# Optimization experiments

Hardware: AMD Instinct MI355X
Metric: run time of the kernel (lower is better)

Reference implementation:

```python
import jax, jax.numpy as jnp
import numpy as np

DIM = 1024
N_HEAD = 16
HEAD_DIM = DIM // N_HEAD
HIDDEN = 4 * DIM
EPS = 1e-6
NEG = -1e9


def setup_inputs() -> dict:
    key = jax.random.key(0)
    ks = jax.random.split(key, 9)
    B, T = 2, 2048
    x = jax.random.normal(ks[0], (B, T, DIM), dtype=jnp.float32)
    # additive causal mask [T, T]
    mask = jnp.where(jnp.tril(jnp.ones((T, T), dtype=bool)), 0.0, NEG).astype(jnp.float32)
    s = 0.02
    wq = jax.random.normal(ks[1], (DIM, DIM), dtype=jnp.float32) * s
    wk = jax.random.normal(ks[2], (DIM, DIM), dtype=jnp.float32) * s
    wv = jax.random.normal(ks[3], (DIM, DIM), dtype=jnp.float32) * s
    wo = jax.random.normal(ks[4], (DIM, DIM), dtype=jnp.float32) * s
    w1 = jax.random.normal(ks[5], (DIM, HIDDEN), dtype=jnp.float32) * s
    w2 = jax.random.normal(ks[6], (HIDDEN, DIM), dtype=jnp.float32) * s
    g_attn = jnp.ones((DIM,), dtype=jnp.float32)
    g_ffn = jnp.ones((DIM,), dtype=jnp.float32)
    return {"x": x, "mask": mask, "wq": wq, "wk": wk, "wv": wv, "wo": wo,
            "w1": w1, "w2": w2, "g_attn": g_attn, "g_ffn": g_ffn}


def _rmsnorm(x, g):
    norm = jax.lax.rsqrt(jnp.mean(jnp.square(x), axis=-1, keepdims=True) + EPS)
    return (x * norm) * g


def _attention(x, mask, wq, wk, wv, wo):
    B, T, C = x.shape
    # project and split heads: [B, H, T, D]
    q = (x @ wq).reshape(B, T, N_HEAD, HEAD_DIM).transpose(0, 2, 1, 3)
    k = (x @ wk).reshape(B, T, N_HEAD, HEAD_DIM).transpose(0, 2, 1, 3)
    v = (x @ wv).reshape(B, T, N_HEAD, HEAD_DIM).transpose(0, 2, 1, 3)
    attn = jnp.einsum('bhtd,bhsd->bhts', q, k) / np.sqrt(HEAD_DIM).astype(np.float32)
    attn = attn + mask  # broadcast [T,T] over [B,H,T,T]
    p = jax.nn.softmax(attn, axis=-1)
    out = jnp.einsum('bhts,bhsd->bhtd', p, v)
    out = out.transpose(0, 2, 1, 3).reshape(B, T, C)
    return out @ wo


def reference(x, mask, wq, wk, wv, wo, w1, w2, g_attn, g_ffn):
    x = x + _attention(_rmsnorm(x, g_attn), mask, wq, wk, wv, wo)
    h = _rmsnorm(x, g_ffn)
    return x + (jax.nn.silu(h @ w1) @ w2)
```

## Files before the change

kernel.cpp:

```cpp
#include <hip/hip_runtime.h>
#include <hip/hip_bf16.h>
#include <cstdint>
#include <cstddef>

#define DIM    1024
#define NHEAD  16
#define HDIM   64
#define HIDDEN 4096
#define TSEQ   2048
#define TOKENS 4096

typedef __attribute__((ext_vector_type(4))) float  f32x4;
typedef __attribute__((ext_vector_type(8))) short  short8;
typedef __attribute__((ext_vector_type(8))) __bf16 bf16x8;

__device__ __forceinline__ short f2bf(float f) {
    union { float f; uint32_t u; } v; v.f = f;
    uint32_t u = v.u;
    uint32_t r = (u + 0x7fffu + ((u >> 16) & 1u)) >> 16;
    return (short)r;
}

__device__ __forceinline__ float bf2f(short s) {
    uint32_t u = ((uint32_t)(uint16_t)s) << 16;
    return __builtin_bit_cast(float, u);
}

__device__ __forceinline__ f32x4 mfma_bf16(short8 a, short8 b, f32x4 c) {
    return __builtin_amdgcn_mfma_f32_16x16x32_bf16(
        __builtin_bit_cast(bf16x8, a), __builtin_bit_cast(bf16x8, b), c, 0, 0, 0);
}

__device__ __forceinline__ void barrier_lds() {
    asm volatile("s_waitcnt lgkmcnt(0)\n\ts_barrier" ::: "memory");
}

__global__ __launch_bounds__(256) void transpose_w(
    const float* __restrict__ W, short* __restrict__ Wt, int K, int N)
{
    __shared__ float tile[64][65];
    const int tid = threadIdx.x;
    const int n0 = blockIdx.x * 64, k0 = blockIdx.y * 64;
    for (int i = tid; i < 4096; i += 256) {
        int r = i >> 6, c = i & 63;
        tile[r][c] = W[(size_t)(k0 + r) * N + n0 + c];
    }
    __syncthreads();
    for (int i = tid; i < 4096; i += 256) {
        int r = i >> 6, c = i & 63;
        Wt[(size_t)(n0 + r) * K + k0 + c] = f2bf(tile[c][r]);
    }
}

__global__ __launch_bounds__(256) void transpose_v(
    const short* __restrict__ qkv, short* __restrict__ Vt)
{
    __shared__ short tile[64][72];
    const int tid = threadIdx.x;
    const int s0 = blockIdx.x * 64, bh = blockIdx.y;
    const int b = bh >> 4, h = bh & 15;
    const short* src = qkv + ((size_t)(b * TSEQ + s0)) * 3072 + 2048 + h * 64;
    for (int i = tid; i < 512; i += 256) {
        int r = i >> 3, cg = i & 7;
        *(short8*)&tile[r][cg * 8] = *(const short8*)(src + (size_t)r * 3072 + cg * 8);
    }
    __syncthreads();
    short* dst = Vt + ((size_t)bh * 64) * TSEQ + s0;
    for (int i = tid; i < 512; i += 256) {
        int d = i >> 3, sg = i & 7;
        short8 o;
#pragma unroll
        for (int j = 0; j < 8; ++j) o[j] = tile[sg * 8 + j][d];
        *(short8*)(dst + (size_t)d * TSEQ + sg * 8) = o;
    }
}

__global__ __launch_bounds__(256) void rmsnorm_k(
    const float* __restrict__ x, const float* __restrict__ g, short* __restrict__ out)
{
    const int t = blockIdx.x, tid = threadIdx.x;
    const int wave = tid >> 6, lane = tid & 63;
    const float4 v = ((const float4*)(x + (size_t)t * DIM))[tid];
    float ss = v.x * v.x + v.y * v.y + v.z * v.z + v.w * v.w;
#pragma unroll
    for (int d = 1; d < 64; d <<= 1) ss += __shfl_xor(ss, d, 64);
    __shared__ float red[4];
    if (lane == 0) red[wave] = ss;
    __syncthreads();
    float tot = red[0] + red[1] + red[2] + red[3];
    float rn = rsqrtf(tot * (1.0f / (float)DIM) + 1e-6f);
    const float4 gv = ((const float4*)g)[tid];
    short4 ov = make_short4(f2bf(v.x * rn * gv.x), f2bf(v.y * rn * gv.y),
                            f2bf(v.z * rn * gv.z), f2bf(v.w * rn * gv.w));
    ((short4*)(out + (size_t)t * DIM))[tid] = ov;
}

template <int EPI>
__global__ __launch_bounds__(256) void gemm_bt(
    const short* __restrict__ A, const short* __restrict__ Bt,
    void* __restrict__ Cout, const float* __restrict__ res,
    int M, int N, int K)
{
    __shared__ short As[128 * 64];
    __shared__ short Bs[128 * 64];
    const int tid  = threadIdx.x;
    const int wave = tid >> 6, lane = tid & 63;
    const int lm = lane & 15, quad = lane >> 4;
    const int wm = wave & 1, wn = wave >> 1;
    const int m0 = blockIdx.x * 128, n0 = blockIdx.y * 128;
    const int Ksl = K / gridDim.z;
    const int kbeg = blockIdx.z * Ksl;
    const int nIter = Ksl >> 6;

    const f32x4 zero = {0.f, 0.f, 0.f, 0.f};
    f32x4 acc[4][4];
#pragma unroll
    for (int i = 0; i < 4; ++i)
#pragma unroll
        for (int j = 0; j < 4; ++j) acc[i][j] = zero;

    const int srow = tid >> 3;
    const int scol = (tid & 7) * 8;
    const int pcol = ((tid & 7) ^ (srow & 7)) * 8;
    const short* Ap = A + (size_t)(m0 + srow) * K + kbeg + scol;
    const short* Bp = Bt + (size_t)(n0 + srow) * K + kbeg + scol;

    short8 ar[4], br[4];

    auto loadtile = [&]() {
#pragma unroll
        for (int j = 0; j < 4; ++j) {
            ar[j] = *(const short8*)(Ap + (size_t)(j * 32) * K);
            br[j] = *(const short8*)(Bp + (size_t)(j * 32) * K);
        }
        Ap += 64; Bp += 64;
    };

    auto storetile = [&]() {
#pragma unroll
        for (int j = 0; j < 4; ++j) {
            *(short8*)&As[(srow + j * 32) * 64 + pcol] = ar[j];
            *(short8*)&Bs[(srow + j * 32) * 64 + pcol] = br[j];
        }
    };

    const int e = lm & 7;
    auto compute = [&]() {
#pragma unroll
        for (int kk = 0; kk < 2; ++kk) {
            short8 af[4], bf[4];
#pragma unroll
            for (int mt = 0; mt < 4; ++mt)
                af[mt] = *(const short8*)&As[(wm * 64 + mt * 16 + lm) * 64 +
                                             ((((kk << 2) | quad) ^ e) << 3)];
#pragma unroll
            for (int nt = 0; nt < 4; ++nt)
                bf[nt] = *(const short8*)&Bs[(wn * 64 + nt * 16 + lm) * 64 +
                                             ((((kk << 2) | quad) ^ e) << 3)];
#pragma unroll
            for (int mt = 0; mt < 4; ++mt)
#pragma unroll
                for (int nt = 0; nt < 4; ++nt)
                    acc[mt][nt] = mfma_bf16(af[mt], bf[nt], acc[mt][nt]);
        }
    };

    loadtile();

    for (int it = 0; it < nIter; ++it) {
        barrier_lds();
        storetile();
        barrier_lds();
        if (it + 1 < nIter) loadtile();
        compute();
    }

#pragma unroll
    for (int mt = 0; mt < 4; ++mt) {
#pragma unroll
        for (int r = 0; r < 4; ++r) {
            const int row = m0 + wm * 64 + mt * 16 + quad * 4 + r;
#pragma unroll
            for (int nt = 0; nt < 4; ++nt) {
                const int col = n0 + wn * 64 + nt * 16 + lm;
                const size_t idx = (size_t)row * N + col;
                const float v = acc[mt][nt][r];
                if constexpr (EPI == 0) {
                    ((short*)Cout)[idx] = f2bf(v);
                } else if constexpr (EPI == 1) {
                    ((float*)Cout)[idx] = res[idx] + v;
                } else if constexpr (EPI == 2) {
                    ((short*)Cout)[idx] = f2bf(v / (1.0f + __expf(-v)));
                } else {
                    ((short*)Cout)[(size_t)blockIdx.z * M * N + idx] = f2bf(v);
                }
            }
        }
    }
}

__global__ __launch_bounds__(256) void combine_k4(
    const short* __restrict__ p, const float* __restrict__ res,
    float* __restrict__ out, int n)
{
    const int i = blockIdx.x * 256 + threadIdx.x;
    if (i * 4 < n) {
        float4 v = ((const float4*)res)[i];
#pragma unroll
        for (int s = 0; s < 4; ++s) {
            short4 ps = ((const short4*)(p + (size_t)s * n))[i];
            v.x += bf2f(ps.x); v.y += bf2f(ps.y);
            v.z += bf2f(ps.z); v.w += bf2f(ps.w);
        }
        ((float4*)out)[i] = v;
    }
}

__global__ __launch_bounds__(256) void combine_rms4(
    const short* __restrict__ p, const float* __restrict__ res,
    const float* __restrict__ g, float* __restrict__ x2out,
    short* __restrict__ nout)
{
    const int t = blockIdx.x, tid = threadIdx.x;
    const int wave = tid >> 6, lane = tid & 63;
    const size_t i4 = (size_t)t * 256 + tid;
    float4 v = ((const float4*)res)[i4];
#pragma unroll
    for (int s = 0; s < 4; ++s) {
        short4 ps = ((const short4*)(p + (size_t)s * TOKENS * DIM))[i4];
        v.x += bf2f(ps.x); v.y += bf2f(ps.y);
        v.z += bf2f(ps.z); v.w += bf2f(ps.w);
    }
    ((float4*)x2out)[i4] = v;
    float ss = v.x * v.x + v.y * v.y + v.z * v.z + v.w * v.w;
#pragma unroll
    for (int d = 1; d < 64; d <<= 1) ss += __shfl_xor(ss, d, 64);
    __shared__ float red[4];
    if (lane == 0) red[wave] = ss;
    __syncthreads();
    float tot = red[0] + red[1] + red[2] + red[3];
    float rn = rsqrtf(tot * (1.0f / (float)DIM) + 1e-6f);
    const float4 gv = ((const float4*)g)[tid];
    short4 ov = make_short4(f2bf(v.x * rn * gv.x), f2bf(v.y * rn * gv.y),
                            f2bf(v.z * rn * gv.z), f2bf(v.w * rn * gv.w));
    ((short4*)nout)[i4] = ov;
}

#define PLP 72
__global__ __launch_bounds__(256, 2) void attn_k(
    const short* __restrict__ qkv, const short* __restrict__ Vt,
    short* __restrict__ out)
{
    __shared__ short Ks[2][64 * 64];
    __shared__ short Vts[2][64 * 64];
    __shared__ short Ps[4][32 * PLP];

    const int tid = threadIdx.x, wave = tid >> 6, lane = tid & 63;
    const int pair = wave >> 1, wv = wave & 1;
    const int lm = lane & 15, quad = lane >> 4;
    const int e = lm & 7;
    const int bh = blockIdx.x;
    const int qt = (gridDim.y - 1) - blockIdx.y;
    const int b = bh >> 4, h = bh & 15;
    const int q0 = qt * 64;

    const int n  = qt + 1;
    const int nA = (n + 1) >> 1;
    const int nP = pair ? (n >> 1) : nA;
    const int sbase = pair ? nA : 0;

    const int tp = tid & 127;
    const int rr = tp >> 3, cg = tp & 7;
    const int pcol = (cg ^ (rr & 7)) * 8;

    const short* qb = qkv + ((size_t)(b * TSEQ + q0)) * 3072 + h * 64;
    short8 aq[2][2];
#pragma unroll
    for (int mt = 0; mt < 2; ++mt)
#pragma unroll
        for (int kk = 0; kk < 2; ++kk)
            aq[mt][kk] = *(const short8*)(qb + (size_t)(wv * 32 + mt * 16 + lm) * 3072 + kk * 32 + quad * 8);

    const short* kb  = qkv + (size_t)b * TSEQ * 3072 + 1024 + h * 64;
    const short* vtb = Vt + (size_t)bh * 64 * TSEQ;

    const short ONEBF = (short)0x3F80;
    const short8 ones8 = {ONEBF, ONEBF, ONEBF, ONEBF, ONEBF, ONEBF, ONEBF, ONEBF};

    const f32x4 zero = {0.f, 0.f, 0.f, 0.f};
    f32x4 o_acc[2][4];
    f32x4 lacc[2];
#pragma unroll
    for (int mt = 0; mt < 2; ++mt) {
#pragma unroll
        for (int t = 0; t < 4; ++t) o_acc[mt][t] = zero;
        lacc[mt] = zero;
    }

    short8 kr[4], vr[4];
    if (nP > 0) {
        const size_t s0i = (size_t)sbase * 64;
#pragma unroll
        for (int j = 0; j < 4; ++j) {
            kr[j] = *(const short8*)(kb + (s0i + rr + j * 16) * 3072 + cg * 8);
            vr[j] = *(const short8*)(vtb + (size_t)(rr + j * 16) * TSEQ + s0i + cg * 8);
        }
    }

    for (int it = 0; it < nA; ++it) {
        const int st = sbase + it;
        const bool act = it < nP;
        __syncthreads();
        if (act) {
#pragma unroll
            for (int j = 0; j < 4; ++j) {
                *(short8*)&Ks[pair][(rr + j * 16) * 64 + pcol] = kr[j];
                *(short8*)&Vts[pair][(rr + j * 16) * 64 + pcol] = vr[j];
            }
        }
        __syncthreads();
        if (act && it + 1 < nP) {
            const size_t sn = (size_t)(st + 1) * 64;
#pragma unroll
            for (int j = 0; j < 4; ++j) {
                kr[j] = *(const short8*)(kb + (sn + rr + j * 16) * 3072 + cg * 8);
                vr[j] = *(const short8*)(vtb + (size_t)(rr + j * 16) * TSEQ + sn + cg * 8);
            }
        }
        if (!act) continue;

        f32x4 sa[2][4];
#pragma unroll
        for (int mt = 0; mt < 2; ++mt)
#pragma unroll
            for (int nt = 0; nt < 4; ++nt) sa[mt][nt] = zero;
#pragma unroll
        for (int kk = 0; kk < 2; ++kk) {
#pragma unroll
            for (int nt = 0; nt < 4; ++nt) {
                short8 bk = *(const short8*)&Ks[pair][(nt * 16 + lm) * 64 +
                                                     ((((kk << 2) | quad) ^ e) << 3)];
                sa[0][nt] = mfma_bf16(aq[0][kk], bk, sa[0][nt]);
                sa[1][nt] = mfma_bf16(aq[1][kk], bk, sa[1][nt]);
            }
        }

        const int s0 = st * 64;
        if (st != qt) {
#pragma unroll
            for (int mt = 0; mt < 2; ++mt)
#pragma unroll
                for (int nt = 0; nt < 4; ++nt)
#pragma unroll
                    for (int r = 0; r < 4; ++r) {
                        float p = exp2f(0.18033688011112042f * sa[mt][nt][r]);
                        Ps[wave][(mt * 16 + quad * 4 + r) * PLP + nt * 16 + lm] =
                            (short)(__builtin_bit_cast(uint32_t, p) >> 16);
                    }
        } else {
#pragma unroll
            for (int mt = 0; mt < 2; ++mt) {
                const int qrow = q0 + wv * 32 + mt * 16 + quad * 4;
#pragma unroll
                for (int nt = 0; nt < 4; ++nt) {
                    const int col = s0 + nt * 16 + lm;
#pragma unroll
                    for (int r = 0; r < 4; ++r) {
                        float p = exp2f(0.18033688011112042f * sa[mt][nt][r]);
                        if (col > qrow + r) p = 0.f;
                        Ps[wave][(mt * 16 + quad * 4 + r) * PLP + nt * 16 + lm] =
                            (short)(__builtin_bit_cast(uint32_t, p) >> 16);
                    }
                }
            }
        }

#pragma unroll
        for (int kk = 0; kk < 2; ++kk) {
            short8 ap0 = *(const short8*)&Ps[wave][lm * PLP + kk * 32 + quad * 8];
            short8 ap1 = *(const short8*)&Ps[wave][(16 + lm) * PLP + kk * 32 + quad * 8];
            lacc[0] = mfma_bf16(ap0, ones8, lacc[0]);
            lacc[1] = mfma_bf16(ap1, ones8, lacc[1]);
#pragma unroll
            for (int t = 0; t < 4; ++t) {
                short8 bv = *(const short8*)&Vts[pair][(t * 16 + lm) * 64 +
                                                       ((((kk << 2) | quad) ^ e) << 3)];
                o_acc[0][t] = mfma_bf16(ap0, bv, o_acc[0][t]);
                o_acc[1][t] = mfma_bf16(ap1, bv, o_acc[1][t]);
            }
        }
    }

    __syncthreads();
    float* Ob = (float*)&Ks[0][0];
    float* Lb = (float*)&Ps[0][0];
    if (pair == 1) {
#pragma unroll
        for (int mt = 0; mt < 2; ++mt)
#pragma unroll
            for (int t = 0; t < 4; ++t)
#pragma unroll
                for (int r = 0; r < 4; ++r)
                    Ob[(wv * 32 + mt * 16 + quad * 4 + r) * 64 + t * 16 + lm] = o_acc[mt][t][r];
        if (lm == 0) {
#pragma unroll
            for (int mt = 0; mt < 2; ++mt)
#pragma unroll
                for (int r = 0; r < 4; ++r)
                    Lb[wv * 32 + mt * 16 + quad * 4 + r] = lacc[mt][r];
        }
    }
    __syncthreads();
    if (pair == 0) {
#pragma unroll
        for (int mt = 0; mt < 2; ++mt) {
#pragma unroll
            for (int r = 0; r < 4; ++r) {
                const int lrow = wv * 32 + mt * 16 + quad * 4 + r;
                float ltot = lacc[mt][r] + Lb[lrow];
                const float inv = 1.0f / ltot;
                const int token = b * TSEQ + q0 + lrow;
#pragma unroll
                for (int t = 0; t < 4; ++t) {
                    float o = o_acc[mt][t][r] + Ob[lrow * 64 + t * 16 + lm];
                    out[(size_t)token * 1024 + h * 64 + t * 16 + lm] = f2bf(o * inv);
                }
            }
        }
    }
}

extern "C" void kernel_launch(void* const* d_in, const int* in_sizes, int n_in,
                              void* d_out, int out_size, void* d_ws, size_t ws_size,
                              hipStream_t stream)
{
    const float* x      = (const float*)d_in[0];
    const float* wq     = (const float*)d_in[2];
    const float* wk     = (const float*)d_in[3];
    const float* wv     = (const float*)d_in[4];
    const float* wo     = (const float*)d_in[5];
    const float* w1     = (const float*)d_in[6];
    const float* w2     = (const float*)d_in[7];
    const float* g_attn = (const float*)d_in[8];
    const float* g_ffn  = (const float*)d_in[9];
    float* out = (float*)d_out;

    char* ws = (char*)d_ws;
    const size_t MB = 1024 * 1024;
    short* Wqkv_t = (short*)(ws + 0);
    short* Wo_t   = (short*)(ws + 6 * MB);
    short* W1_t   = (short*)(ws + 8 * MB);
    short* xn     = (short*)(ws + 16 * MB);
    short* hbuf   = (short*)(ws + 24 * MB);
    short* qkv    = (short*)(ws + 32 * MB);
    short* pbufO  = (short*)(ws + 32 * MB);
    short* Vt     = (short*)(ws + 64 * MB);
    float* x2     = (float*)(ws + 64 * MB);
    short* W2_t   = (short*)(ws + 80 * MB);
    short* pbuf2  = (short*)(ws + 0);

    dim3 blk(256);

    transpose_w<<<dim3(16, 16), blk, 0, stream>>>(wq, Wqkv_t, 1024, 1024);
    transpose_w<<<dim3(16, 16), blk, 0, stream>>>(wk, Wqkv_t + (size_t)1024 * 1024, 1024, 1024);
    transpose_w<<<dim3(16, 16), blk, 0, stream>>>(wv, Wqkv_t + (size_t)2048 * 1024, 1024, 1024);
    transpose_w<<<dim3(16, 16), blk, 0, stream>>>(wo, Wo_t, 1024, 1024);
    transpose_w<<<dim3(64, 16), blk, 0, stream>>>(w1, W1_t, 1024, 4096);
    transpose_w<<<dim3(16, 64), blk, 0, stream>>>(w2, W2_t, 4096, 1024);

    rmsnorm_k<<<TOKENS, blk, 0, stream>>>(x, g_attn, xn);

    gemm_bt<0><<<dim3(TOKENS / 128, 3072 / 128), blk, 0, stream>>>(
        xn, Wqkv_t, qkv, nullptr, TOKENS, 3072, 1024);

    transpose_v<<<dim3(TSEQ / 64, 32), blk, 0, stream>>>(qkv, Vt);

    attn_k<<<dim3(32, TSEQ / 64), dim3(256), 0, stream>>>(qkv, Vt, xn);

    gemm_bt<3><<<dim3(TOKENS / 128, 1024 / 128, 4), blk, 0, stream>>>(
        xn, Wo_t, pbufO, nullptr, TOKENS, 1024, 1024);

    combine_rms4<<<TOKENS, blk, 0, stream>>>(pbufO, x, g_ffn, x2, hbuf);

    gemm_bt<2><<<dim3(TOKENS / 128, HIDDEN / 128), blk, 0, stream>>>(
        hbuf, W1_t, qkv, nullptr, TOKENS, HIDDEN, 1024);

    gemm_bt<3><<<dim3(TOKENS / 128, 1024 / 128, 4), blk, 0, stream>>>(
        qkv, W2_t, pbuf2, nullptr, TOKENS, 1024, HIDDEN);

    combine_k4<<<dim3(TOKENS * DIM / 4 / 256), blk, 0, stream>>>(
        pbuf2, x2, out, TOKENS * DIM);
}
```

Baseline: 355.4 us.

## Use 256x256-tile 8-wave GEMM with direct-to-LDS loads for W2 projection

```diff
diff --git a/kernel.cpp b/kernel.cpp
--- a/kernel.cpp
+++ b/kernel.cpp
@@ -34,6 +34,16 @@
 __device__ __forceinline__ void barrier_lds() {
     asm volatile("s_waitcnt lgkmcnt(0)\n\ts_barrier" ::: "memory");
 }
+
+__device__ __forceinline__ void glds16(const short* g, short* l) {
+    __builtin_amdgcn_global_load_lds(
+        (const __attribute__((address_space(1))) void*)g,
+        (__attribute__((address_space(3))) void*)l,
+        16, 0, 0);
+}
+
+#define BARX()  asm volatile("s_barrier" ::: "memory")
+#define LGKM0() asm volatile("s_waitcnt lgkmcnt(0)" ::: "memory")
 
 __global__ __launch_bounds__(256) void transpose_w(
     const float* __restrict__ W, short* __restrict__ Wt, int K, int N)
@@ -199,6 +209,119 @@
     }
 }
 
+template <int EPI>
+__global__ __launch_bounds__(512, 2) void gemm8_bt(
+    const short* __restrict__ A, const short* __restrict__ Bt,
+    void* __restrict__ Cout, const float* __restrict__ res,
+    int M, int N, int K)
+{
+    __shared__ short As[2][256 * 64];
+    __shared__ short Bs[2][256 * 64];
+    const int tid  = threadIdx.x;
+    const int wave = tid >> 6, lane = tid & 63;
+    const int lm = lane & 15, quad = lane >> 4;
+    const int ex = lm & 7;
+    const int wm = wave & 1, wn = wave >> 1;
+    const int m0 = blockIdx.x * 256, n0 = blockIdx.y * 256;
+    const int Ksl = K / gridDim.z;
+    const int kbeg = blockIdx.z * Ksl;
+    const int T = Ksl >> 6;
+
+    const f32x4 zero = {0.f, 0.f, 0.f, 0.f};
+    f32x4 acc[8][4];
+#pragma unroll
+    for (int i = 0; i < 8; ++i)
+#pragma unroll
+        for (int j = 0; j < 4; ++j) acc[i][j] = zero;
+
+    const int srow = wave * 8 + (lane >> 3);
+    const int scol = ((lane & 7) ^ ((lane >> 3) & 7)) * 8;
+    const short* ApS = A + (size_t)(m0 + srow) * K + kbeg + scol;
+    const short* BpS = Bt + (size_t)(n0 + srow) * K + kbeg + scol;
+
+    auto stageA = [&](int buf) {
+#pragma unroll
+        for (int j = 0; j < 4; ++j)
+            glds16(ApS + (size_t)(j * 64) * K, &As[buf][(j * 64 + wave * 8) * 64]);
+        ApS += 64;
+    };
+    auto stageB = [&](int buf) {
+#pragma unroll
+        for (int j = 0; j < 4; ++j)
+            glds16(BpS + (size_t)(j * 64) * K, &Bs[buf][(j * 64 + wave * 8) * 64]);
+        BpS += 64;
+    };
+
+#define READ_A(buf, kk) do { _Pragma("unroll") \
+    for (int mt = 0; mt < 8; ++mt) \
+        af[mt] = *(const short8*)&As[buf][(wm * 128 + mt * 16 + lm) * 64 + \
+                                          ((((kk) << 2) | quad) ^ ex) * 8]; } while (0)
+#define READ_B(buf, kk, np) do { _Pragma("unroll") \
+    for (int j = 0; j < 2; ++j) \
+        bfp[j] = *(const short8*)&Bs[buf][(wn * 64 + ((np) * 2 + j) * 16 + lm) * 64 + \
+                                          ((((kk) << 2) | quad) ^ ex) * 8]; } while (0)
+#define MFMA16(np) do { _Pragma("unroll") \
+    for (int mt = 0; mt < 8; ++mt) { \
+        acc[mt][(np) * 2 + 0] = mfma_bf16(af[mt], bfp[0], acc[mt][(np) * 2 + 0]); \
+        acc[mt][(np) * 2 + 1] = mfma_bf16(af[mt], bfp[1], acc[mt][(np) * 2 + 1]); \
+    } } while (0)
+
+    stageA(0); stageB(0); stageA(1);
+    asm volatile("s_waitcnt vmcnt(4)" ::: "memory");
+    BARX();
+
+    for (int t = 0; t < T; ++t) {
+        const int buf = t & 1;
+        short8 af[8], bfp[2];
+        READ_A(buf, 0); READ_B(buf, 0, 0);
+        if (t + 1 < T) stageB(buf ^ 1);
+        BARX(); LGKM0();
+        __builtin_amdgcn_s_setprio(1); MFMA16(0); __builtin_amdgcn_s_setprio(0);
+        BARX();
+        READ_B(buf, 0, 1);
+        BARX(); LGKM0();
+        __builtin_amdgcn_s_setprio(1); MFMA16(1); __builtin_amdgcn_s_setprio(0);
+        BARX();
+        READ_A(buf, 1); READ_B(buf, 1, 0);
+        BARX(); LGKM0();
+        __builtin_amdgcn_s_setprio(1); MFMA16(0); __builtin_amdgcn_s_setprio(0);
+        BARX();
+        READ_B(buf, 1, 1);
+        if (t + 2 < T) stageA(buf);
+        BARX(); LGKM0();
+        __builtin_amdgcn_s_setprio(1); MFMA16(1); __builtin_amdgcn_s_setprio(0);
+        if (t + 2 < T) { asm volatile("s_waitcnt vmcnt(4)" ::: "memory"); }
+        else           { asm volatile("s_waitcnt vmcnt(0)" ::: "memory"); }
+        BARX();
+    }
+#undef READ_A
+#undef READ_B
+#undef MFMA16
+
+#pragma unroll
+    for (int mt = 0; mt < 8; ++mt) {
+#pragma unroll
+        for (int r = 0; r < 4; ++r) {
+            const int row = m0 + wm * 128 + mt * 16 + quad * 4 + r;
+#pragma unroll
+            for (int nt = 0; nt < 4; ++nt) {
+                const int col = n0 + wn * 64 + nt * 16 + lm;
+                const size_t idx = (size_t)row * N + col;
+                const float v = acc[mt][nt][r];
+                if constexpr (EPI == 0) {
+                    ((short*)Cout)[idx] = f2bf(v);
+                } else if constexpr (EPI == 1) {
+                    ((float*)Cout)[idx] = res[idx] + v;
+                } else if constexpr (EPI == 2) {
+                    ((short*)Cout)[idx] = f2bf(v / (1.0f + __expf(-v)));
+                } else {
+                    ((short*)Cout)[(size_t)blockIdx.z * M * N + idx] = f2bf(v);
+                }
+            }
+        }
+    }
+}
+
 __global__ __launch_bounds__(256) void combine_k4(
     const short* __restrict__ p, const float* __restrict__ res,
     float* __restrict__ out, int n)
@@ -485,7 +608,7 @@
     gemm_bt<2><<<dim3(TOKENS / 128, HIDDEN / 128), blk, 0, stream>>>(
         hbuf, W1_t, qkv, nullptr, TOKENS, HIDDEN, 1024);
 
-    gemm_bt<3><<<dim3(TOKENS / 128, 1024 / 128, 4), blk, 0, stream>>>(
+    gemm8_bt<3><<<dim3(TOKENS / 256, 1024 / 256, 4), dim3(512), 0, stream>>>(
         qkv, W2_t, pbuf2, nullptr, TOKENS, 1024, HIDDEN);
 
     combine_k4<<<dim3(TOKENS * DIM / 4 / 256), blk, 0, stream>>>(
```

Result: no change. 351.3 us (-1.1%).
